# Kernel tuning notes

Measured on AMD Instinct MI355X. Metric: run time of the kernel, lower is better.

The kernel has to match this reference:

```python
import jax, jax.numpy as jnp
import numpy as np

EPS = 1e-6  # flax nnx LayerNorm default

def _ln(x):
    # LayerNorm without scale/bias
    m = jnp.mean(x, axis=-1, keepdims=True)
    v = jnp.mean(jnp.square(x - m), axis=-1, keepdims=True)
    return (x - m) * jax.lax.rsqrt(v + EPS)

def _modulate(x, shift, scale):
    return x * (1.0 + scale[:, None]) + shift[:, None]

def setup_inputs() -> dict:
    key = jax.random.key(0)
    B, S, H, NH = 8, 1024, 1024, 16
    ks = jax.random.split(key, 12)
    s = lambda k, sh: jax.random.normal(k, sh, dtype=jnp.float32) * 0.02
    return {
        "x": jax.random.normal(ks[0], (B, S, H), dtype=jnp.float32),
        "c": jax.random.normal(ks[1], (B, H), dtype=jnp.float32),
        "w_ada": s(ks[2], (H, 6 * H)),
        "b_ada": jnp.zeros((6 * H,), dtype=jnp.float32),
        "w_qkv": s(ks[3], (H, 3 * H)),
        "w_proj": s(ks[4], (H, H)),
        "b_proj": jnp.zeros((H,), dtype=jnp.float32),
        "w_mlp1": s(ks[5], (H, 4 * H)),
        "b_mlp1": jnp.zeros((4 * H,), dtype=jnp.float32),
        "w_mlp2": s(ks[6], (4 * H, H)),
        "b_mlp2": jnp.zeros((H,), dtype=jnp.float32),
    }

def reference(x, c, w_ada, b_ada, w_qkv, w_proj, b_proj, w_mlp1, b_mlp1, w_mlp2, b_mlp2):
    B, S, H = x.shape
    NH = 16
    CH = H // NH
    # adaLN modulation: silu -> Linear
    cmod = jax.nn.silu(c) @ w_ada + b_ada  # [B, 6H]
    shift_msa, scale_msa, gate_msa, shift_mlp, scale_mlp, gate_mlp = jnp.split(cmod, 6, axis=-1)
    # attention branch
    x_mod = _modulate(_ln(x), shift_msa, scale_msa)
    qkv = x_mod @ w_qkv  # [B, S, 3H]
    k, q, v = jnp.split(qkv, 3, axis=-1)  # note source order: k, q, v
    k = k.reshape(B, S, NH, CH)
    q = q.reshape(B, S, NH, CH)
    v = v.reshape(B, S, NH, CH)
    q = q / CH  # faithful: divide by head_dim (not sqrt)
    w = jnp.einsum('bqhc,bkhc->bhqk', q, k).astype(jnp.float32)
    w = jax.nn.softmax(w, axis=-1)
    y = jnp.einsum('bhqk,bkhc->bqhc', w, v).reshape(B, S, H)
    attn_x = y @ w_proj + b_proj
    x = x + gate_msa[:, None] * attn_x
    # MLP branch
    x_mod2 = _modulate(_ln(x), shift_mlp, scale_mlp)
    h = jax.nn.gelu(x_mod2 @ w_mlp1 + b_mlp1)
    mlp_x = h @ w_mlp2 + b_mlp2
    x = x + gate_mlp[:, None] * mlp_x
    return x
```

## Files before the change

### kernel.cpp

```cpp
#include <hip/hip_runtime.h>
#include <stdint.h>

typedef unsigned short u16;
using bf16x8 = __attribute__((ext_vector_type(8))) __bf16;
using f32x4  = __attribute__((ext_vector_type(4))) float;

#define MFMA16(a,b,c) __builtin_amdgcn_mfma_f32_16x16x32_bf16((a),(b),(c),0,0,0)

__device__ __forceinline__ u16 f2bf(float f) {
  union { float f; uint32_t u; } v; v.f = f;
  uint32_t r = v.u + 0x7FFFu + ((v.u >> 16) & 1u);
  return (u16)(r >> 16);
}

__device__ __forceinline__ void gload_lds16(const void* g, void* l) {
  typedef const __attribute__((address_space(1))) void* gp_t;
  typedef __attribute__((address_space(3))) void* lp_t;
  __builtin_amdgcn_global_load_lds((gp_t)(uintptr_t)g,
                                   (lp_t)(uint32_t)(uintptr_t)l, 16, 0, 0);
}

__global__ __launch_bounds__(256)
void adaln_part_k(const float* __restrict__ c, const float* __restrict__ w,
                  float* __restrict__ partial) {
  const int jb = blockIdx.x, ks = blockIdx.y;
  const int j = jb * 256 + threadIdx.x;
  __shared__ float sil[8][32];
  {
    int b = threadIdx.x >> 5, kk = threadIdx.x & 31;
    float v = c[b * 1024 + ks * 32 + kk];
    sil[b][kk] = v / (1.f + __expf(-v));
  }
  __syncthreads();
  float acc[8] = {0,0,0,0,0,0,0,0};
#pragma unroll 8
  for (int kk = 0; kk < 32; ++kk) {
    float wv = w[(size_t)(ks * 32 + kk) * 6144 + j];
#pragma unroll
    for (int b = 0; b < 8; ++b) acc[b] += sil[b][kk] * wv;
  }
#pragma unroll
  for (int b = 0; b < 8; ++b)
    partial[((size_t)ks * 8 + b) * 6144 + j] = acc[b];
}

__global__ __launch_bounds__(256)
void adaln_red_k(const float* __restrict__ partial, const float* __restrict__ bias,
                 float* __restrict__ cmod) {
  int g = blockIdx.x * 256 + threadIdx.x;
  int j = g % 6144;
  float s = bias[j];
#pragma unroll 8
  for (int ks = 0; ks < 32; ++ks)
    s += partial[(size_t)ks * 8 * 6144 + g];
  cmod[g] = s;
}

__global__ __launch_bounds__(256)
void tcast_k(const float* __restrict__ in, u16* __restrict__ out, int K, int N,
             int lo, int hi, float scale) {
  __shared__ u16 t[64][65];
  int n0 = blockIdx.x * 64, k0 = blockIdx.y * 64;
#pragma unroll
  for (int i = 0; i < 16; ++i) {
    int idx = i * 256 + threadIdx.x;
    int r = idx >> 6, cc = idx & 63;
    float v = in[(size_t)(k0 + r) * N + n0 + cc];
    int n = n0 + cc;
    if (n >= lo && n < hi) v *= scale;
    t[r][cc] = f2bf(v);
  }
  __syncthreads();
#pragma unroll
  for (int i = 0; i < 16; ++i) {
    int idx = i * 256 + threadIdx.x;
    int r = idx >> 6, cc = idx & 63;
    out[(size_t)(n0 + r) * K + k0 + cc] = t[cc][r];
  }
}

__global__ __launch_bounds__(256)
void lnmod_k(const float* __restrict__ x, const float* __restrict__ cmod,
             int shift_off, int scale_off, u16* __restrict__ out) {
  int row = blockIdx.x;
  int b = row >> 10;
  const float4* xr = (const float4*)(x + (size_t)row * 1024);
  float4 v = xr[threadIdx.x];
  float s = v.x + v.y + v.z + v.w;
  float sq = v.x * v.x + v.y * v.y + v.z * v.z + v.w * v.w;
#pragma unroll
  for (int m = 32; m >= 1; m >>= 1) {
    s  += __shfl_xor(s, m);
    sq += __shfl_xor(sq, m);
  }
  __shared__ float ss[4], ssq[4];
  int wave = threadIdx.x >> 6, lane = threadIdx.x & 63;
  if (lane == 0) { ss[wave] = s; ssq[wave] = sq; }
  __syncthreads();
  s  = ss[0] + ss[1] + ss[2] + ss[3];
  sq = ssq[0] + ssq[1] + ssq[2] + ssq[3];
  float mean = s * (1.f / 1024.f);
  float var  = sq * (1.f / 1024.f) - mean * mean;
  float rstd = rsqrtf(var + 1e-6f);
  int col = threadIdx.x * 4;
  const float* sh = cmod + (size_t)b * 6144 + shift_off + col;
  const float* sc = cmod + (size_t)b * 6144 + scale_off + col;
  float xv[4] = {v.x, v.y, v.z, v.w};
  union { u16 o[4]; uint64_t u; } pk;
#pragma unroll
  for (int j = 0; j < 4; ++j)
    pk.o[j] = f2bf((xv[j] - mean) * rstd * (1.f + sc[j]) + sh[j]);
  *(uint64_t*)(out + (size_t)row * 1024 + col) = pk.u;
}

__global__ __launch_bounds__(256)
void tv_k(const u16* __restrict__ qkv, u16* __restrict__ vt) {
  __shared__ u16 t[64][65];
  int r0 = blockIdx.x * 64;
  int h = blockIdx.y;
  int b = r0 >> 10;
  int s0 = r0 & 1023;
#pragma unroll
  for (int i = 0; i < 16; ++i) {
    int idx = i * 256 + threadIdx.x;
    int r = idx >> 6, cc = idx & 63;
    t[r][cc] = qkv[(size_t)(r0 + r) * 3072 + 2048 + h * 64 + cc];
  }
  __syncthreads();
#pragma unroll
  for (int i = 0; i < 16; ++i) {
    int idx = i * 256 + threadIdx.x;
    int ch = idx >> 6, scc = idx & 63;
    vt[((size_t)(b * 16 + h) * 64 + ch) * 1024 + s0 + scc] = t[scc][ch];
  }
}

__device__ __forceinline__ float gelu_f(float x) {
  float z = 1.5957691216057308f * (x + 0.044715f * x * x * x);
  return x / (1.f + __expf(-z));
}

template <int EP>
__global__ __launch_bounds__(256)
void gemm_k(const u16* __restrict__ A, const u16* __restrict__ Bt,
            int N, int K,
            const float* __restrict__ bias, const float* __restrict__ resid,
            const float* __restrict__ gate, void* __restrict__ outp) {
  __shared__ __align__(16) u16 lds[2][2][128 * 32];
  const int bn = blockIdx.x, bm = blockIdx.y;
  const int tid = threadIdx.x;
  const int wave = tid >> 6, lane = tid & 63;
  const int l15 = lane & 15, lhi = lane >> 4;
  const int wr = wave >> 1, wc = wave & 1;
  f32x4 acc[4][4] = {};
  const int nkt = K >> 5;
  const size_t arow0 = (size_t)bm * 128;
  const size_t brow0 = (size_t)bn * 128;

  auto stage = [&](int buf, int kt) {
#pragma unroll
    for (int i = 0; i < 2; ++i) {
      int c = (i * 4 + wave) * 64 + lane;
      int row = c >> 2, kc = c & 3;
      gload_lds16(A  + (arow0 + row) * K + (size_t)kt * 32 + kc * 8,
                  &lds[buf][0][(i * 4 + wave) * 512]);
      gload_lds16(Bt + (brow0 + row) * K + (size_t)kt * 32 + kc * 8,
                  &lds[buf][1][(i * 4 + wave) * 512]);
    }
  };

  stage(0, 0);
  __syncthreads();
  for (int kt = 0; kt < nkt; ++kt) {
    int cur = kt & 1;
    if (kt + 1 < nkt) stage(cur ^ 1, kt + 1);
    bf16x8 af[4], bfr[4];
#pragma unroll
    for (int m = 0; m < 4; ++m)
      af[m] = *(const bf16x8*)&lds[cur][0][(wr * 64 + m * 16 + l15) * 32 + lhi * 8];
#pragma unroll
    for (int n = 0; n < 4; ++n)
      bfr[n] = *(const bf16x8*)&lds[cur][1][(wc * 64 + n * 16 + l15) * 32 + lhi * 8];
#pragma unroll
    for (int m = 0; m < 4; ++m)
#pragma unroll
      for (int n = 0; n < 4; ++n)
        acc[m][n] = MFMA16(af[m], bfr[n], acc[m][n]);
    __syncthreads();
  }

#pragma unroll
  for (int m = 0; m < 4; ++m) {
    int row = bm * 128 + wr * 64 + m * 16 + lhi * 4;
#pragma unroll
    for (int n = 0; n < 4; ++n) {
      int col = bn * 128 + wc * 64 + n * 16 + l15;
#pragma unroll
      for (int r = 0; r < 4; ++r) {
        int rr = row + r;
        float v = acc[m][n][r];
        if (EP == 0) {
          ((u16*)outp)[(size_t)rr * N + col] = f2bf(v);
        } else if (EP == 1) {
          ((u16*)outp)[(size_t)rr * N + col] = f2bf(gelu_f(v + bias[col]));
        } else {
          float t = v + bias[col];
          int b = rr >> 10;
          float res = resid[(size_t)rr * N + col];
          ((float*)outp)[(size_t)rr * N + col] = res + gate[(size_t)b * 6144 + col] * t;
        }
      }
    }
  }
}

__global__ __launch_bounds__(256)
void attn_k(const u16* __restrict__ qkv, const u16* __restrict__ vt,
            u16* __restrict__ y) {
  const int qt = blockIdx.x, h = blockIdx.y, b = blockIdx.z;
  const int tid = threadIdx.x, wave = tid >> 6, lane = tid & 63;
  const int l15 = lane & 15, lhi = lane >> 4;
  __shared__ __align__(16) u16 Qs[64 * 64];
  __shared__ __align__(16) u16 Ks[2][64 * 64];
  __shared__ __align__(16) u16 Vs[2][64 * 64];
  __shared__ __align__(16) u16 Ps[64 * 64];
  const size_t qrow0 = (size_t)b * 1024 + qt * 64;
  const size_t krow0 = (size_t)b * 1024;
  const size_t vrow0 = (size_t)(b * 16 + h) * 64;

  auto stageQ = [&]() {
#pragma unroll
    for (int i = 0; i < 2; ++i) {
      int c = (i * 4 + wave) * 64 + lane;
      int r = c >> 3, j = (c & 7) ^ (c >> 3 & 7);
      gload_lds16(qkv + (qrow0 + r) * 3072 + 1024 + h * 64 + j * 8,
                  &Qs[(i * 4 + wave) * 512]);
    }
  };
  auto stageKV = [&](int buf, int kt) {
#pragma unroll
    for (int i = 0; i < 2; ++i) {
      int c = (i * 4 + wave) * 64 + lane;
      int r = c >> 3, j = (c & 7) ^ (c >> 3 & 7);
      gload_lds16(qkv + (krow0 + kt * 64 + r) * 3072 + h * 64 + j * 8,
                  &Ks[buf][(i * 4 + wave) * 512]);
      gload_lds16(vt + (vrow0 + r) * 1024 + kt * 64 + j * 8,
                  &Vs[buf][(i * 4 + wave) * 512]);
    }
  };
  auto ldb = [](const u16* base, int row, int cc) -> bf16x8 {
    return *(const bf16x8*)&base[row * 64 + ((cc ^ (row & 7)) << 3)];
  };

  stageQ();
  stageKV(0, 0);
  __syncthreads();
  bf16x8 qf[2];
  qf[0] = ldb(Qs, wave * 16 + l15, lhi);
  qf[1] = ldb(Qs, wave * 16 + l15, 4 + lhi);

  bf16x8 ones;
#pragma unroll
  for (int j = 0; j < 8; ++j) ones[j] = (__bf16)1.0f;

  float m_r[4];
  f32x4 o[5] = {};
#pragma unroll
  for (int r = 0; r < 4; ++r) m_r[r] = -3.0e38f;

  for (int kt = 0; kt < 16; ++kt) {
    int cur = kt & 1;
    if (kt < 15) stageKV(cur ^ 1, kt + 1);
    f32x4 sf[4] = {};
    __builtin_amdgcn_s_setprio(1);
#pragma unroll
    for (int n = 0; n < 4; ++n) {
      bf16x8 k0 = ldb(Ks[cur], n * 16 + l15, lhi);
      bf16x8 k1 = ldb(Ks[cur], n * 16 + l15, 4 + lhi);
      sf[n] = MFMA16(qf[0], k0, sf[n]);
      sf[n] = MFMA16(qf[1], k1, sf[n]);
    }
    __builtin_amdgcn_s_setprio(0);
#pragma unroll
    for (int r = 0; r < 4; ++r) {
      float mx = fmaxf(fmaxf(sf[0][r], sf[1][r]), fmaxf(sf[2][r], sf[3][r]));
      mx = fmaxf(mx, __shfl_xor(mx, 1));
      mx = fmaxf(mx, __shfl_xor(mx, 2));
      mx = fmaxf(mx, __shfl_xor(mx, 4));
      mx = fmaxf(mx, __shfl_xor(mx, 8));
      float mn = fmaxf(m_r[r], mx);
      float al = __expf(m_r[r] - mn);
      m_r[r] = mn;
      float p0 = __expf(sf[0][r] - mn);
      float p1 = __expf(sf[1][r] - mn);
      float p2 = __expf(sf[2][r] - mn);
      float p3 = __expf(sf[3][r] - mn);
      o[0][r] *= al; o[1][r] *= al; o[2][r] *= al; o[3][r] *= al; o[4][r] *= al;
      int row = wave * 16 + lhi * 4 + r;
      int rb = row * 64, sw = (row & 7) << 3;
      Ps[rb + (l15 ^ sw)]        = f2bf(p0);
      Ps[rb + ((l15 + 16) ^ sw)] = f2bf(p1);
      Ps[rb + ((l15 + 32) ^ sw)] = f2bf(p2);
      Ps[rb + ((l15 + 48) ^ sw)] = f2bf(p3);
    }
    bf16x8 pf0 = ldb(Ps, wave * 16 + l15, lhi);
    bf16x8 pf1 = ldb(Ps, wave * 16 + l15, 4 + lhi);
    __builtin_amdgcn_s_setprio(1);
#pragma unroll
    for (int n = 0; n < 4; ++n) {
      bf16x8 v0 = ldb(Vs[cur], n * 16 + l15, lhi);
      bf16x8 v1 = ldb(Vs[cur], n * 16 + l15, 4 + lhi);
      o[n] = MFMA16(pf0, v0, o[n]);
      o[n] = MFMA16(pf1, v1, o[n]);
    }
    o[4] = MFMA16(pf0, ones, o[4]);
    o[4] = MFMA16(pf1, ones, o[4]);
    __builtin_amdgcn_s_setprio(0);
    __syncthreads();
  }
#pragma unroll
  for (int r = 0; r < 4; ++r) {
    float inv = 1.0f / o[4][r];
    size_t yrow = (qrow0 + wave * 16 + lhi * 4 + r) * 1024 + h * 64 + l15;
    y[yrow]      = f2bf(o[0][r] * inv);
    y[yrow + 16] = f2bf(o[1][r] * inv);
    y[yrow + 32] = f2bf(o[2][r] * inv);
    y[yrow + 48] = f2bf(o[3][r] * inv);
  }
}

extern "C" void kernel_launch(void* const* d_in, const int* in_sizes, int n_in,
                              void* d_out, int out_size, void* d_ws, size_t ws_size,
                              hipStream_t stream) {
  const float* x      = (const float*)d_in[0];
  const float* c      = (const float*)d_in[1];
  const float* w_ada  = (const float*)d_in[2];
  const float* b_ada  = (const float*)d_in[3];
  const float* w_qkv  = (const float*)d_in[4];
  const float* w_proj = (const float*)d_in[5];
  const float* b_proj = (const float*)d_in[6];
  const float* w_mlp1 = (const float*)d_in[7];
  const float* b_mlp1 = (const float*)d_in[8];
  const float* w_mlp2 = (const float*)d_in[9];
  const float* b_mlp2 = (const float*)d_in[10];
  float* out = (float*)d_out;

  char* ws = (char*)d_ws;
  size_t off = 0;
  auto alloc = [&](size_t bytes) {
    void* p = ws + off;
    off += (bytes + 255) & ~(size_t)255;
    return p;
  };
  float* cmod  = (float*)alloc((size_t)8 * 6144 * 4);
  float* apart = (float*)alloc((size_t)32 * 8 * 6144 * 4);
  u16* wqkvT   = (u16*)alloc((size_t)3072 * 1024 * 2);
  u16* wprojT  = (u16*)alloc((size_t)1024 * 1024 * 2);
  u16* wmlp1T  = (u16*)alloc((size_t)4096 * 1024 * 2);
  u16* wmlp2T  = (u16*)alloc((size_t)1024 * 4096 * 2);
  u16* xmod    = (u16*)alloc((size_t)8192 * 1024 * 2);
  u16* qkv     = (u16*)alloc((size_t)8192 * 3072 * 2);
  u16* vt      = (u16*)alloc((size_t)8 * 16 * 64 * 1024 * 2);
  float* x1    = (float*)alloc((size_t)8192 * 1024 * 4);
  u16* hbuf    = (u16*)alloc((size_t)8192 * 4096 * 2);
  u16* ybuf  = xmod;
  u16* xmod2 = qkv;

  adaln_part_k<<<dim3(24, 32), 256, 0, stream>>>(c, w_ada, apart);
  adaln_red_k<<<192, 256, 0, stream>>>(apart, b_ada, cmod);
  tcast_k<<<dim3(3072 / 64, 1024 / 64), 256, 0, stream>>>(w_qkv,  wqkvT,  1024, 3072,
                                                          1024, 2048, 1.0f / 64.0f);
  tcast_k<<<dim3(1024 / 64, 1024 / 64), 256, 0, stream>>>(w_proj, wprojT, 1024, 1024, 0, 0, 1.f);
  tcast_k<<<dim3(4096 / 64, 1024 / 64), 256, 0, stream>>>(w_mlp1, wmlp1T, 1024, 4096, 0, 0, 1.f);
  tcast_k<<<dim3(1024 / 64, 4096 / 64), 256, 0, stream>>>(w_mlp2, wmlp2T, 4096, 1024, 0, 0, 1.f);
  lnmod_k<<<8192, 256, 0, stream>>>(x, cmod, 0, 1024, xmod);
  gemm_k<0><<<dim3(3072 / 128, 8192 / 128), 256, 0, stream>>>(
      xmod, wqkvT, 3072, 1024, nullptr, nullptr, nullptr, qkv);
  tv_k<<<dim3(128, 16), 256, 0, stream>>>(qkv, vt);
  attn_k<<<dim3(16, 16, 8), 256, 0, stream>>>(qkv, vt, ybuf);
  gemm_k<2><<<dim3(1024 / 128, 8192 / 128), 256, 0, stream>>>(
      ybuf, wprojT, 1024, 1024, b_proj, x, cmod + 2048, x1);
  lnmod_k<<<8192, 256, 0, stream>>>(x1, cmod, 3072, 4096, xmod2);
  gemm_k<1><<<dim3(4096 / 128, 8192 / 128), 256, 0, stream>>>(
      xmod2, wmlp1T, 4096, 1024, b_mlp1, nullptr, nullptr, hbuf);
  gemm_k<2><<<dim3(1024 / 128, 8192 / 128), 256, 0, stream>>>(
      hbuf, wmlp2T, 1024, 4096, b_mlp2, x1, cmod + 5120, out);
}
```

Before: 434.9 us.

## Enlarge GEMM tiles to 256x128x64 with triple-buffered swizzled LDS pipeline

The GEMM kernel moves to 512 threads (8 waves) with a 256x128 output tile and K-step of 64. It uses three LDS buffers with prefetch two stages ahead, guarded by explicit vmcnt waits. An XOR swizzle on LDS chunks avoids bank conflicts, and s_setprio is raised around the MFMA block. The aim is to improve operand reuse, overlap global loads with compute, and cut barrier count, at the cost of more LDS (~144KB per block) and register pressure, plus fragile hand-written waitcnt counts.

```diff
diff --git a/kernel.cpp b/kernel.cpp
--- a/kernel.cpp
+++ b/kernel.cpp
@@ -141,57 +141,89 @@
 }
 
 template <int EP>
-__global__ __launch_bounds__(256)
+__global__ __launch_bounds__(512, 2)
 void gemm_k(const u16* __restrict__ A, const u16* __restrict__ Bt,
             int N, int K,
             const float* __restrict__ bias, const float* __restrict__ resid,
             const float* __restrict__ gate, void* __restrict__ outp) {
-  __shared__ __align__(16) u16 lds[2][2][128 * 32];
+  __shared__ __align__(16) u16 Asb[3][256 * 64];
+  __shared__ __align__(16) u16 Bsb[3][128 * 64];
   const int bn = blockIdx.x, bm = blockIdx.y;
   const int tid = threadIdx.x;
   const int wave = tid >> 6, lane = tid & 63;
   const int l15 = lane & 15, lhi = lane >> 4;
   const int wr = wave >> 1, wc = wave & 1;
+  const int nkt = K >> 6;
+  const size_t arow0 = (size_t)bm * 256;
+  const size_t brow0 = (size_t)bn * 128;
+
   f32x4 acc[4][4] = {};
-  const int nkt = K >> 5;
-  const size_t arow0 = (size_t)bm * 128;
-  const size_t brow0 = (size_t)bn * 128;
 
   auto stage = [&](int buf, int kt) {
+    const u16* ab = A  + arow0 * K + (size_t)kt * 64;
+    const u16* bb = Bt + brow0 * K + (size_t)kt * 64;
+#pragma unroll
+    for (int i = 0; i < 4; ++i) {
+      int q = i * 512 + tid;
+      int r = q >> 3, c = (q & 7) ^ (r & 7);
+      gload_lds16(ab + (size_t)r * K + c * 8, &Asb[buf][(i * 8 + wave) * 512]);
+    }
 #pragma unroll
     for (int i = 0; i < 2; ++i) {
-      int c = (i * 4 + wave) * 64 + lane;
-      int row = c >> 2, kc = c & 3;
-      gload_lds16(A  + (arow0 + row) * K + (size_t)kt * 32 + kc * 8,
-                  &lds[buf][0][(i * 4 + wave) * 512]);
-      gload_lds16(Bt + (brow0 + row) * K + (size_t)kt * 32 + kc * 8,
-                  &lds[buf][1][(i * 4 + wave) * 512]);
+      int q = i * 512 + tid;
+      int r = q >> 3, c = (q & 7) ^ (r & 7);
+      gload_lds16(bb + (size_t)r * K + c * 8, &Bsb[buf][(i * 8 + wave) * 512]);
     }
   };
 
   stage(0, 0);
-  __syncthreads();
-  for (int kt = 0; kt < nkt; ++kt) {
-    int cur = kt & 1;
-    if (kt + 1 < nkt) stage(cur ^ 1, kt + 1);
-    bf16x8 af[4], bfr[4];
-#pragma unroll
-    for (int m = 0; m < 4; ++m)
-      af[m] = *(const bf16x8*)&lds[cur][0][(wr * 64 + m * 16 + l15) * 32 + lhi * 8];
-#pragma unroll
-    for (int n = 0; n < 4; ++n)
-      bfr[n] = *(const bf16x8*)&lds[cur][1][(wc * 64 + n * 16 + l15) * 32 + lhi * 8];
-#pragma unroll
-    for (int m = 0; m < 4; ++m)
-#pragma unroll
-      for (int n = 0; n < 4; ++n)
-        acc[m][n] = MFMA16(af[m], bfr[n], acc[m][n]);
-    __syncthreads();
+  if (nkt > 1) stage(1, 1);
+  asm volatile("s_waitcnt vmcnt(6)" ::: "memory");
+  __syncthreads();
+
+  for (int t = 0; t < nkt; ++t) {
+    const int s = t % 3;
+    if (t + 2 < nkt) stage((t + 2) % 3, t + 2);
+
+    bf16x8 af[4][2], bfr[4][2];
+#pragma unroll
+    for (int m = 0; m < 4; ++m) {
+      int r = wr * 64 + m * 16 + l15;
+#pragma unroll
+      for (int kh = 0; kh < 2; ++kh) {
+        int c = (kh * 4 + lhi) ^ (r & 7);
+        af[m][kh] = *(const bf16x8*)&Asb[s][r * 64 + c * 8];
+      }
+    }
+#pragma unroll
+    for (int n = 0; n < 4; ++n) {
+      int r = wc * 64 + n * 16 + l15;
+#pragma unroll
+      for (int kh = 0; kh < 2; ++kh) {
+        int c = (kh * 4 + lhi) ^ (r & 7);
+        bfr[n][kh] = *(const bf16x8*)&Bsb[s][r * 64 + c * 8];
+      }
+    }
+    __builtin_amdgcn_s_setprio(1);
+#pragma unroll
+    for (int kh = 0; kh < 2; ++kh)
+#pragma unroll
+      for (int m = 0; m < 4; ++m)
+#pragma unroll
+        for (int n = 0; n < 4; ++n)
+          acc[m][n] = MFMA16(af[m][kh], bfr[n][kh], acc[m][n]);
+    __builtin_amdgcn_s_setprio(0);
+
+    if (t + 1 < nkt) {
+      if (t + 2 < nkt) asm volatile("s_waitcnt vmcnt(6)" ::: "memory");
+      else             asm volatile("s_waitcnt vmcnt(0)" ::: "memory");
+      __syncthreads();
+    }
   }
 
 #pragma unroll
   for (int m = 0; m < 4; ++m) {
-    int row = bm * 128 + wr * 64 + m * 16 + lhi * 4;
+    int row = bm * 256 + wr * 64 + m * 16 + lhi * 4;
 #pragma unroll
     for (int n = 0; n < 4; ++n) {
       int col = bn * 128 + wc * 64 + n * 16 + l15;
@@ -204,10 +236,10 @@
         } else if (EP == 1) {
           ((u16*)outp)[(size_t)rr * N + col] = f2bf(gelu_f(v + bias[col]));
         } else {
-          float t = v + bias[col];
+          float t2 = v + bias[col];
           int b = rr >> 10;
           float res = resid[(size_t)rr * N + col];
-          ((float*)outp)[(size_t)rr * N + col] = res + gate[(size_t)b * 6144 + col] * t;
+          ((float*)outp)[(size_t)rr * N + col] = res + gate[(size_t)b * 6144 + col] * t2;
         }
       }
     }
@@ -374,15 +406,15 @@
   tcast_k<<<dim3(4096 / 64, 1024 / 64), 256, 0, stream>>>(w_mlp1, wmlp1T, 1024, 4096, 0, 0, 1.f);
   tcast_k<<<dim3(1024 / 64, 4096 / 64), 256, 0, stream>>>(w_mlp2, wmlp2T, 4096, 1024, 0, 0, 1.f);
   lnmod_k<<<8192, 256, 0, stream>>>(x, cmod, 0, 1024, xmod);
-  gemm_k<0><<<dim3(3072 / 128, 8192 / 128), 256, 0, stream>>>(
+  gemm_k<0><<<dim3(3072 / 128, 8192 / 256), 512, 0, stream>>>(
       xmod, wqkvT, 3072, 1024, nullptr, nullptr, nullptr, qkv);
   tv_k<<<dim3(128, 16), 256, 0, stream>>>(qkv, vt);
   attn_k<<<dim3(16, 16, 8), 256, 0, stream>>>(qkv, vt, ybuf);
-  gemm_k<2><<<dim3(1024 / 128, 8192 / 128), 256, 0, stream>>>(
+  gemm_k<2><<<dim3(1024 / 128, 8192 / 256), 512, 0, stream>>>(
       ybuf, wprojT, 1024, 1024, b_proj, x, cmod + 2048, x1);
   lnmod_k<<<8192, 256, 0, stream>>>(x1, cmod, 3072, 4096, xmod2);
-  gemm_k<1><<<dim3(4096 / 128, 8192 / 128), 256, 0, stream>>>(
+  gemm_k<1><<<dim3(4096 / 128, 8192 / 256), 512, 0, stream>>>(
       xmod2, wmlp1T, 4096, 1024, b_mlp1, nullptr, nullptr, hbuf);
-  gemm_k<2><<<dim3(1024 / 128, 8192 / 128), 256, 0, stream>>>(
+  gemm_k<2><<<dim3(1024 / 128, 8192 / 256), 512, 0, stream>>>(
       hbuf, wmlp2T, 1024, 4096, b_mlp2, x1, cmod + 5120, out);
 }
```

New measurement: 417.3 us. -4.0%, faster.
